# Performance work log

Measured on AMD Instinct MI355X. Metric: run time of the kernel, lower is better.

## Reference

```python
import jax, jax.numpy as jnp
import numpy as np

V, E, H, C, L, S, NL = 50257, 512, 1024, 1024, 1024, 2048, 2


def setup_inputs() -> dict:
    key = jax.random.key(0)
    ks = jax.random.split(key, 28)
    w = 0.02  # weight init scale
    def n(k, shape, s=1.0):
        return jax.random.normal(k, shape, dtype=jnp.float32) * s
    return {
        'input_ids': jax.random.randint(ks[0], (1,), 0, V, dtype=jnp.int32),
        'h0': n(ks[1], (NL, 1, H)),
        'c0': n(ks[2], (NL, 1, H)),
        'left_context': n(ks[3], (S, C)),
        'right_context': n(ks[4], (S, C)),
        'lemma_outputs': n(ks[5], (S, L)),
        # parameters
        'embedding': n(ks[6], (V, E), w),
        'W_ih0': n(ks[7], (4 * H, E), w), 'W_hh0': n(ks[8], (4 * H, H), w),
        'b_ih0': n(ks[9], (4 * H,), w), 'b_hh0': n(ks[10], (4 * H,), w),
        'W_ih1': n(ks[11], (4 * H, H), w), 'W_hh1': n(ks[12], (4 * H, H), w),
        'b_ih1': n(ks[13], (4 * H,), w), 'b_hh1': n(ks[14], (4 * H,), w),
        'W_left': n(ks[15], (H, C), w), 'b_left': n(ks[16], (H,), w),
        'W_right': n(ks[17], (H, C), w), 'b_right': n(ks[18], (H,), w),
        'W_lemma': n(ks[19], (H, L), w), 'b_lemma': n(ks[20], (H,), w),
        'W_concat': n(ks[21], (H, H + 2 * C + L), w), 'b_concat': n(ks[22], (H,), w),
        'W_out': n(ks[23], (V, H), w), 'b_out': n(ks[24], (V,), w),
    }


def _lstm_step(x, h, c, W_ih, W_hh, b_ih, b_hh):
    # torch LSTM gate order: i, f, g, o
    g = x @ W_ih.T + b_ih + h @ W_hh.T + b_hh  # [1, 4H]
    i, f, gg, o = jnp.split(g, 4, axis=-1)
    i = jax.nn.sigmoid(i); f = jax.nn.sigmoid(f)
    gg = jnp.tanh(gg); o = jax.nn.sigmoid(o)
    c_new = f * c + i * gg
    h_new = o * jnp.tanh(c_new)
    return h_new, c_new


def _attend(ctx, W, b, q):
    # ctx: [S, C], q: [1, H] -> Luong-style attention
    e = (ctx @ W.T + b) @ q.T          # [S, 1]
    a = jax.nn.softmax(e[:, 0])        # [S]
    return (a @ ctx)[None, :]          # [1, C]


def reference(input_ids, h0, c0, left_context, right_context, lemma_outputs,
              embedding, W_ih0, W_hh0, b_ih0, b_hh0, W_ih1, W_hh1, b_ih1, b_hh1,
              W_left, b_left, W_right, b_right, W_lemma, b_lemma,
              W_concat, b_concat, W_out, b_out):
    x = embedding[input_ids]  # [1, E]  (dropout p=0 -> identity)
    h_0, c_0 = _lstm_step(x, h0[0], c0[0], W_ih0, W_hh0, b_ih0, b_hh0)
    h_1, c_1 = _lstm_step(h_0, h0[1], c0[1], W_ih1, W_hh1, b_ih1, b_hh1)
    rnn_output = h_1  # [1, H]
    lcontext = _attend(left_context, W_left, b_left, rnn_output)
    rcontext = _attend(right_context, W_right, b_right, rnn_output)
    lemma_ctx = _attend(lemma_outputs, W_lemma, b_lemma, rnn_output)
    concat_in = jnp.concatenate([rnn_output, lcontext, rcontext, lemma_ctx], axis=-1)
    concat_out = jnp.tanh(concat_in @ W_concat.T + b_concat)  # [1, H]
    output = concat_out @ W_out.T + b_out                      # [1, V]
    h_new = jnp.stack([h_0, h_1], axis=0)  # [NL, 1, H]
    c_new = jnp.stack([c_0, c_1], axis=0)
    return output, h_new, c_new
```

## Files before the change

### kernel.cpp

```cpp
#include <hip/hip_runtime.h>
#include <hip/hip_bf16.h>
#include <math.h>


#define WS_H0        0
#define WS_CONCAT_IN 1024
#define WS_CTXOUT    2048
#define WS_V         5120
#define WS_E         8192
#define WS_COUT      20480
#define OUT_V        50257

__device__ __forceinline__ float wave_sum(float v) {
#pragma unroll
    for (int o = 32; o > 0; o >>= 1) v += __shfl_down(v, o, 64);
    return v;
}

__device__ __forceinline__ float dot4(float4 a, float4 b) {
    return a.x * b.x + a.y * b.y + a.z * b.z + a.w * b.w;
}

__device__ __forceinline__ float sigmoidf_(float x) {
    return 1.0f / (1.0f + expf(-x));
}

__global__ __launch_bounds__(256) void lstm_kernel(
    const float* __restrict__ x_base, const int* __restrict__ ids, int E_in,
    const float* __restrict__ W_ih, const float* __restrict__ W_hh,
    const float* __restrict__ b_ih, const float* __restrict__ b_hh,
    const float* __restrict__ hprev, const float* __restrict__ cprev,
    float* __restrict__ h_ws, float* __restrict__ h_out, float* __restrict__ c_out,
    float* __restrict__ zero_base, int zero_count)
{
    if (zero_base != nullptr) {
        int idx = blockIdx.x * 256 + threadIdx.x;
        if (idx < zero_count) zero_base[idx] = 0.0f;
    }

    const float* x = (ids != nullptr) ? (x_base + (size_t)512 * (size_t)ids[0]) : x_base;

    const int k = blockIdx.x;
    const int w = threadIdx.x >> 6;
    const int lane = threadIdx.x & 63;
    const int row = w * 1024 + k;

    float acc = 0.0f;
    {
        const float4* r4 = (const float4*)(W_ih + (size_t)row * E_in);
        const float4* x4 = (const float4*)x;
        const int n4 = E_in >> 2;
        for (int i = lane; i < n4; i += 64) acc += dot4(r4[i], x4[i]);
    }
    {
        const float4* r4 = (const float4*)(W_hh + (size_t)row * 1024);
        const float4* h4 = (const float4*)hprev;
        for (int i = lane; i < 256; i += 64) acc += dot4(r4[i], h4[i]);
    }
    acc = wave_sum(acc);

    __shared__ float g[4];
    if (lane == 0) g[w] = acc + b_ih[row] + b_hh[row];
    __syncthreads();
    if (threadIdx.x == 0) {
        float i_ = sigmoidf_(g[0]);
        float f_ = sigmoidf_(g[1]);
        float g_ = tanhf(g[2]);
        float o_ = sigmoidf_(g[3]);
        float c_new = f_ * cprev[k] + i_ * g_;
        float h_new = o_ * tanhf(c_new);
        h_ws[k] = h_new;
        h_out[k] = h_new;
        c_out[k] = c_new;
    }
}

__global__ __launch_bounds__(256) void attn_v_kernel(
    const float* __restrict__ W0, const float* __restrict__ W1,
    const float* __restrict__ W2, const float* __restrict__ q,
    float* __restrict__ v)
{
    const int a = blockIdx.x >> 6;
    const int chunk = blockIdx.x & 63;
    const float* W = (a == 0) ? W0 : (a == 1) ? W1 : W2;
    const int c = threadIdx.x * 4;
    float4 acc = make_float4(0.f, 0.f, 0.f, 0.f);
    const int h0 = chunk * 16;
#pragma unroll 4
    for (int h = h0; h < h0 + 16; ++h) {
        float qh = q[h];
        float4 wv = *(const float4*)(W + (size_t)h * 1024 + c);
        acc.x += wv.x * qh; acc.y += wv.y * qh;
        acc.z += wv.z * qh; acc.w += wv.w * qh;
    }
    float* vd = v + a * 1024 + c;
    atomicAdd(vd + 0, acc.x); atomicAdd(vd + 1, acc.y);
    atomicAdd(vd + 2, acc.z); atomicAdd(vd + 3, acc.w);
}

__global__ __launch_bounds__(256) void attn_e_kernel(
    const float* __restrict__ C0, const float* __restrict__ C1,
    const float* __restrict__ C2, const float* __restrict__ v,
    float* __restrict__ e)
{
    const int wid = (blockIdx.x * 256 + threadIdx.x) >> 6;
    const int lane = threadIdx.x & 63;
    if (wid >= 3 * 2048) return;
    const int a = wid >> 11;
    const int s = wid & 2047;
    const float* ctx = (a == 0) ? C0 : (a == 1) ? C1 : C2;
    const float4* r4 = (const float4*)(ctx + (size_t)s * 1024);
    const float4* v4 = (const float4*)(v + a * 1024);
    float acc = 0.0f;
    for (int i = lane; i < 256; i += 64) acc += dot4(r4[i], v4[i]);
    acc = wave_sum(acc);
    if (lane == 0) e[a * 2048 + s] = acc;
}

__global__ __launch_bounds__(256) void attn_ctx_kernel(
    const float* __restrict__ C0, const float* __restrict__ C1,
    const float* __restrict__ C2, const float* __restrict__ e,
    float* __restrict__ ctx_out)
{
    const int a = blockIdx.x >> 6;
    const int chunk = blockIdx.x & 63;
    const float* ctx = (a == 0) ? C0 : (a == 1) ? C1 : C2;
    const float* ea = e + a * 2048;

    __shared__ float red[256];
    const int t = threadIdx.x;
    float m = -1e30f;
    for (int i = t; i < 2048; i += 256) m = fmaxf(m, ea[i]);
    red[t] = m; __syncthreads();
    for (int o = 128; o > 0; o >>= 1) {
        if (t < o) red[t] = fmaxf(red[t], red[t + o]);
        __syncthreads();
    }
    m = red[0]; __syncthreads();

    float ssum = 0.0f;
    for (int i = t; i < 2048; i += 256) ssum += expf(ea[i] - m);
    red[t] = ssum; __syncthreads();
    for (int o = 128; o > 0; o >>= 1) {
        if (t < o) red[t] += red[t + o];
        __syncthreads();
    }
    const float inv = 1.0f / red[0];

    const int c = t * 4;
    float4 acc = make_float4(0.f, 0.f, 0.f, 0.f);
    const int s0 = chunk * 32;
    for (int s = s0; s < s0 + 32; ++s) {
        float wgt = expf(ea[s] - m) * inv;
        float4 cv = *(const float4*)(ctx + (size_t)s * 1024 + c);
        acc.x += wgt * cv.x; acc.y += wgt * cv.y;
        acc.z += wgt * cv.z; acc.w += wgt * cv.w;
    }
    float* od = ctx_out + a * 1024 + c;
    atomicAdd(od + 0, acc.x); atomicAdd(od + 1, acc.y);
    atomicAdd(od + 2, acc.z); atomicAdd(od + 3, acc.w);
}

__global__ __launch_bounds__(256) void concat_kernel(
    const float* __restrict__ W, const float* __restrict__ b,
    const float* __restrict__ cin, float* __restrict__ cout)
{
    const int w = threadIdx.x >> 6;
    const int lane = threadIdx.x & 63;
    const int j = blockIdx.x * 4 + w;
    const float4* r4 = (const float4*)(W + (size_t)j * 4096);
    const float4* x4 = (const float4*)cin;
    float acc = 0.0f;
    for (int i = lane; i < 1024; i += 64) acc += dot4(r4[i], x4[i]);
    acc = wave_sum(acc);
    if (lane == 0) cout[j] = tanhf(acc + b[j]);
}

__global__ __launch_bounds__(256) void out_kernel(
    const float* __restrict__ W, const float* __restrict__ b,
    const float* __restrict__ x, float* __restrict__ out)
{
    const int wid = (blockIdx.x * 256 + threadIdx.x) >> 6;
    const int lane = threadIdx.x & 63;
    const int nwaves = gridDim.x * 4;
    const float4* x4 = (const float4*)x;
    for (int vrow = wid; vrow < OUT_V; vrow += nwaves) {
        const float4* r4 = (const float4*)(W + (size_t)vrow * 1024);
        float acc = 0.0f;
        for (int i = lane; i < 256; i += 64) acc += dot4(r4[i], x4[i]);
        acc = wave_sum(acc);
        if (lane == 0) out[vrow] = acc + b[vrow];
    }
}

extern "C" void kernel_launch(void* const* d_in, const int* in_sizes, int n_in,
                              void* d_out, int out_size, void* d_ws, size_t ws_size,
                              hipStream_t stream) {
    const int*   input_ids = (const int*)  d_in[0];
    const float* h0        = (const float*)d_in[1];
    const float* c0        = (const float*)d_in[2];
    const float* lctx      = (const float*)d_in[3];
    const float* rctx      = (const float*)d_in[4];
    const float* lemma     = (const float*)d_in[5];
    const float* emb       = (const float*)d_in[6];
    const float* W_ih0     = (const float*)d_in[7];
    const float* W_hh0     = (const float*)d_in[8];
    const float* b_ih0     = (const float*)d_in[9];
    const float* b_hh0     = (const float*)d_in[10];
    const float* W_ih1     = (const float*)d_in[11];
    const float* W_hh1     = (const float*)d_in[12];
    const float* b_ih1     = (const float*)d_in[13];
    const float* b_hh1     = (const float*)d_in[14];
    const float* W_left    = (const float*)d_in[15];
    const float* b_left    = (const float*)d_in[16];
    const float* W_right   = (const float*)d_in[17];
    const float* W_lemma   = (const float*)d_in[19];
    const float* W_concat  = (const float*)d_in[21];
    const float* b_concat  = (const float*)d_in[22];
    const float* W_out     = (const float*)d_in[23];
    const float* b_out     = (const float*)d_in[24];
    (void)b_left; (void)in_sizes; (void)n_in; (void)out_size; (void)ws_size;

    float* out = (float*)d_out;
    float* ws  = (float*)d_ws;

    float* h0_out = out + OUT_V;
    float* h1_out = out + OUT_V + 1024;
    float* c0_out = out + OUT_V + 2048;
    float* c1_out = out + OUT_V + 3072;

    lstm_kernel<<<1024, 256, 0, stream>>>(
        emb, input_ids, 512, W_ih0, W_hh0, b_ih0, b_hh0,
        h0, c0, ws + WS_H0, h0_out, c0_out,
        ws + WS_CTXOUT, 6144 );

    lstm_kernel<<<1024, 256, 0, stream>>>(
        ws + WS_H0, nullptr, 1024, W_ih1, W_hh1, b_ih1, b_hh1,
        h0 + 1024, c0 + 1024, ws + WS_CONCAT_IN, h1_out, c1_out,
        nullptr, 0);

    attn_v_kernel<<<192, 256, 0, stream>>>(
        W_left, W_right, W_lemma, ws + WS_CONCAT_IN, ws + WS_V);

    attn_e_kernel<<<1536, 256, 0, stream>>>(
        lctx, rctx, lemma, ws + WS_V, ws + WS_E);

    attn_ctx_kernel<<<192, 256, 0, stream>>>(
        lctx, rctx, lemma, ws + WS_E, ws + WS_CTXOUT);

    concat_kernel<<<256, 256, 0, stream>>>(
        W_concat, b_concat, ws + WS_CONCAT_IN, ws + WS_COUT);

    out_kernel<<<2048, 256, 0, stream>>>(
        W_out, b_out, ws + WS_COUT, out);
}
```

Measured before the change: 466.0 us.

## Fuse all decoder stages into one cooperative persistent kernel with grid syncs

```diff
diff --git a/kernel.cpp b/kernel.cpp
--- a/kernel.cpp
+++ b/kernel.cpp
@@ -1,15 +1,23 @@
 #include <hip/hip_runtime.h>
 #include <hip/hip_bf16.h>
+#include <hip/hip_cooperative_groups.h>
 #include <math.h>
 
-
-#define WS_H0        0
-#define WS_CONCAT_IN 1024
-#define WS_CTXOUT    2048
-#define WS_V         5120
-#define WS_E         8192
-#define WS_COUT      20480
-#define OUT_V        50257
+namespace cg = cooperative_groups;
+
+
+#define NV 50257
+#define GRID 512
+
+struct Params {
+    const int* ids;
+    const float *h0, *c0, *lctx, *rctx, *lemma, *emb;
+    const float *W_ih0, *W_hh0, *b_ih0, *b_hh0;
+    const float *W_ih1, *W_hh1, *b_ih1, *b_hh1;
+    const float *W_left, *W_right, *W_lemma;
+    const float *W_concat, *b_concat, *W_out, *b_out;
+    float *out, *ws;
+};
 
 __device__ __forceinline__ float wave_sum(float v) {
 #pragma unroll
@@ -25,232 +33,244 @@
     return 1.0f / (1.0f + expf(-x));
 }
 
-__global__ __launch_bounds__(256) void lstm_kernel(
-    const float* __restrict__ x_base, const int* __restrict__ ids, int E_in,
-    const float* __restrict__ W_ih, const float* __restrict__ W_hh,
-    const float* __restrict__ b_ih, const float* __restrict__ b_hh,
-    const float* __restrict__ hprev, const float* __restrict__ cprev,
-    float* __restrict__ h_ws, float* __restrict__ h_out, float* __restrict__ c_out,
-    float* __restrict__ zero_base, int zero_count)
-{
-    if (zero_base != nullptr) {
-        int idx = blockIdx.x * 256 + threadIdx.x;
-        if (idx < zero_count) zero_base[idx] = 0.0f;
-    }
-
-    const float* x = (ids != nullptr) ? (x_base + (size_t)512 * (size_t)ids[0]) : x_base;
-
-    const int k = blockIdx.x;
-    const int w = threadIdx.x >> 6;
-    const int lane = threadIdx.x & 63;
-    const int row = w * 1024 + k;
-
-    float acc = 0.0f;
-    {
-        const float4* r4 = (const float4*)(W_ih + (size_t)row * E_in);
-        const float4* x4 = (const float4*)x;
-        const int n4 = E_in >> 2;
-        for (int i = lane; i < n4; i += 64) acc += dot4(r4[i], x4[i]);
-    }
-    {
-        const float4* r4 = (const float4*)(W_hh + (size_t)row * 1024);
-        const float4* h4 = (const float4*)hprev;
-        for (int i = lane; i < 256; i += 64) acc += dot4(r4[i], h4[i]);
-    }
-    acc = wave_sum(acc);
+__global__ __launch_bounds__(256, 2) void fused_decoder(Params p) {
+    cg::grid_group grid = cg::this_grid();
+    const int bid  = blockIdx.x;
+    const int tid  = threadIdx.x;
+    const int w    = tid >> 6;
+    const int lane = tid & 63;
+
+    float* h0_ws = p.ws;
+    float* cin   = p.ws + 1024;
+    float* vbuf  = p.ws + 5120;
+    float* ebuf  = p.ws + 8192;
+    float* cout  = p.ws + 14336;
+    float* h_out = p.out + NV;
+    float* c_out = p.out + NV + 2048;
 
     __shared__ float g[4];
-    if (lane == 0) g[w] = acc + b_ih[row] + b_hh[row];
-    __syncthreads();
-    if (threadIdx.x == 0) {
-        float i_ = sigmoidf_(g[0]);
-        float f_ = sigmoidf_(g[1]);
-        float g_ = tanhf(g[2]);
-        float o_ = sigmoidf_(g[3]);
-        float c_new = f_ * cprev[k] + i_ * g_;
-        float h_new = o_ * tanhf(c_new);
-        h_ws[k] = h_new;
-        h_out[k] = h_new;
-        c_out[k] = c_new;
-    }
-}
-
-__global__ __launch_bounds__(256) void attn_v_kernel(
-    const float* __restrict__ W0, const float* __restrict__ W1,
-    const float* __restrict__ W2, const float* __restrict__ q,
-    float* __restrict__ v)
-{
-    const int a = blockIdx.x >> 6;
-    const int chunk = blockIdx.x & 63;
-    const float* W = (a == 0) ? W0 : (a == 1) ? W1 : W2;
-    const int c = threadIdx.x * 4;
-    float4 acc = make_float4(0.f, 0.f, 0.f, 0.f);
-    const int h0 = chunk * 16;
+    __shared__ float red[256];
+
+    if (bid < 24) {
+        p.ws[2048 + bid * 256 + tid] = 0.0f;
+    }
+    {
+        const float* x = p.emb + (size_t)512 * (size_t)p.ids[0];
+        for (int k = bid; k < 1024; k += GRID) {
+            const int row = w * 1024 + k;
+            float acc = 0.0f;
+            {
+                const float4* r4 = (const float4*)(p.W_ih0 + (size_t)row * 512);
+                const float4* x4 = (const float4*)x;
+#pragma unroll
+                for (int j = 0; j < 2; ++j) acc += dot4(r4[lane + 64 * j], x4[lane + 64 * j]);
+            }
+            {
+                const float4* r4 = (const float4*)(p.W_hh0 + (size_t)row * 1024);
+                const float4* h4 = (const float4*)p.h0;
+#pragma unroll
+                for (int j = 0; j < 4; ++j) acc += dot4(r4[lane + 64 * j], h4[lane + 64 * j]);
+            }
+            acc = wave_sum(acc);
+            if (lane == 0) g[w] = acc + p.b_ih0[row] + p.b_hh0[row];
+            __syncthreads();
+            if (tid == 0) {
+                float i_ = sigmoidf_(g[0]);
+                float f_ = sigmoidf_(g[1]);
+                float g_ = tanhf(g[2]);
+                float o_ = sigmoidf_(g[3]);
+                float c_new = f_ * p.c0[k] + i_ * g_;
+                float h_new = o_ * tanhf(c_new);
+                h0_ws[k]  = h_new;
+                h_out[k]  = h_new;
+                c_out[k]  = c_new;
+            }
+            __syncthreads();
+        }
+    }
+    grid.sync();
+
+    {
+        for (int k = bid; k < 1024; k += GRID) {
+            const int row = w * 1024 + k;
+            float acc = 0.0f;
+            {
+                const float4* r4 = (const float4*)(p.W_ih1 + (size_t)row * 1024);
+                const float4* x4 = (const float4*)h0_ws;
+#pragma unroll
+                for (int j = 0; j < 4; ++j) acc += dot4(r4[lane + 64 * j], x4[lane + 64 * j]);
+            }
+            {
+                const float4* r4 = (const float4*)(p.W_hh1 + (size_t)row * 1024);
+                const float4* h4 = (const float4*)(p.h0 + 1024);
+#pragma unroll
+                for (int j = 0; j < 4; ++j) acc += dot4(r4[lane + 64 * j], h4[lane + 64 * j]);
+            }
+            acc = wave_sum(acc);
+            if (lane == 0) g[w] = acc + p.b_ih1[row] + p.b_hh1[row];
+            __syncthreads();
+            if (tid == 0) {
+                float i_ = sigmoidf_(g[0]);
+                float f_ = sigmoidf_(g[1]);
+                float g_ = tanhf(g[2]);
+                float o_ = sigmoidf_(g[3]);
+                float c_new = f_ * p.c0[1024 + k] + i_ * g_;
+                float h_new = o_ * tanhf(c_new);
+                cin[k]          = h_new;
+                h_out[1024 + k] = h_new;
+                c_out[1024 + k] = c_new;
+            }
+            __syncthreads();
+        }
+    }
+    grid.sync();
+
+    if (bid < 192) {
+        const int a = bid >> 6;
+        const int chunk = bid & 63;
+        const float* W = (a == 0) ? p.W_left : (a == 1) ? p.W_right : p.W_lemma;
+        const int c = tid * 4;
+        float4 acc = make_float4(0.f, 0.f, 0.f, 0.f);
 #pragma unroll 4
-    for (int h = h0; h < h0 + 16; ++h) {
-        float qh = q[h];
-        float4 wv = *(const float4*)(W + (size_t)h * 1024 + c);
-        acc.x += wv.x * qh; acc.y += wv.y * qh;
-        acc.z += wv.z * qh; acc.w += wv.w * qh;
-    }
-    float* vd = v + a * 1024 + c;
-    atomicAdd(vd + 0, acc.x); atomicAdd(vd + 1, acc.y);
-    atomicAdd(vd + 2, acc.z); atomicAdd(vd + 3, acc.w);
-}
-
-__global__ __launch_bounds__(256) void attn_e_kernel(
-    const float* __restrict__ C0, const float* __restrict__ C1,
-    const float* __restrict__ C2, const float* __restrict__ v,
-    float* __restrict__ e)
-{
-    const int wid = (blockIdx.x * 256 + threadIdx.x) >> 6;
-    const int lane = threadIdx.x & 63;
-    if (wid >= 3 * 2048) return;
-    const int a = wid >> 11;
-    const int s = wid & 2047;
-    const float* ctx = (a == 0) ? C0 : (a == 1) ? C1 : C2;
-    const float4* r4 = (const float4*)(ctx + (size_t)s * 1024);
-    const float4* v4 = (const float4*)(v + a * 1024);
-    float acc = 0.0f;
-    for (int i = lane; i < 256; i += 64) acc += dot4(r4[i], v4[i]);
-    acc = wave_sum(acc);
-    if (lane == 0) e[a * 2048 + s] = acc;
-}
-
-__global__ __launch_bounds__(256) void attn_ctx_kernel(
-    const float* __restrict__ C0, const float* __restrict__ C1,
-    const float* __restrict__ C2, const float* __restrict__ e,
-    float* __restrict__ ctx_out)
-{
-    const int a = blockIdx.x >> 6;
-    const int chunk = blockIdx.x & 63;
-    const float* ctx = (a == 0) ? C0 : (a == 1) ? C1 : C2;
-    const float* ea = e + a * 2048;
-
-    __shared__ float red[256];
-    const int t = threadIdx.x;
-    float m = -1e30f;
-    for (int i = t; i < 2048; i += 256) m = fmaxf(m, ea[i]);
-    red[t] = m; __syncthreads();
-    for (int o = 128; o > 0; o >>= 1) {
-        if (t < o) red[t] = fmaxf(red[t], red[t + o]);
-        __syncthreads();
-    }
-    m = red[0]; __syncthreads();
-
-    float ssum = 0.0f;
-    for (int i = t; i < 2048; i += 256) ssum += expf(ea[i] - m);
-    red[t] = ssum; __syncthreads();
-    for (int o = 128; o > 0; o >>= 1) {
-        if (t < o) red[t] += red[t + o];
-        __syncthreads();
-    }
-    const float inv = 1.0f / red[0];
-
-    const int c = t * 4;
-    float4 acc = make_float4(0.f, 0.f, 0.f, 0.f);
-    const int s0 = chunk * 32;
-    for (int s = s0; s < s0 + 32; ++s) {
-        float wgt = expf(ea[s] - m) * inv;
-        float4 cv = *(const float4*)(ctx + (size_t)s * 1024 + c);
-        acc.x += wgt * cv.x; acc.y += wgt * cv.y;
-        acc.z += wgt * cv.z; acc.w += wgt * cv.w;
-    }
-    float* od = ctx_out + a * 1024 + c;
-    atomicAdd(od + 0, acc.x); atomicAdd(od + 1, acc.y);
-    atomicAdd(od + 2, acc.z); atomicAdd(od + 3, acc.w);
-}
-
-__global__ __launch_bounds__(256) void concat_kernel(
-    const float* __restrict__ W, const float* __restrict__ b,
-    const float* __restrict__ cin, float* __restrict__ cout)
-{
-    const int w = threadIdx.x >> 6;
-    const int lane = threadIdx.x & 63;
-    const int j = blockIdx.x * 4 + w;
-    const float4* r4 = (const float4*)(W + (size_t)j * 4096);
-    const float4* x4 = (const float4*)cin;
-    float acc = 0.0f;
-    for (int i = lane; i < 1024; i += 64) acc += dot4(r4[i], x4[i]);
-    acc = wave_sum(acc);
-    if (lane == 0) cout[j] = tanhf(acc + b[j]);
-}
-
-__global__ __launch_bounds__(256) void out_kernel(
-    const float* __restrict__ W, const float* __restrict__ b,
-    const float* __restrict__ x, float* __restrict__ out)
-{
-    const int wid = (blockIdx.x * 256 + threadIdx.x) >> 6;
-    const int lane = threadIdx.x & 63;
-    const int nwaves = gridDim.x * 4;
-    const float4* x4 = (const float4*)x;
-    for (int vrow = wid; vrow < OUT_V; vrow += nwaves) {
-        const float4* r4 = (const float4*)(W + (size_t)vrow * 1024);
+        for (int h = chunk * 16; h < chunk * 16 + 16; ++h) {
+            float qh = cin[h];
+            float4 wv = *(const float4*)(W + (size_t)h * 1024 + c);
+            acc.x += wv.x * qh; acc.y += wv.y * qh;
+            acc.z += wv.z * qh; acc.w += wv.w * qh;
+        }
+        float* vd = vbuf + a * 1024 + c;
+        atomicAdd(vd + 0, acc.x); atomicAdd(vd + 1, acc.y);
+        atomicAdd(vd + 2, acc.z); atomicAdd(vd + 3, acc.w);
+    }
+    grid.sync();
+
+    {
+        const int wid = bid * 4 + w;
+        for (int rr = wid; rr < 6144; rr += GRID * 4) {
+            const int a = rr >> 11;
+            const int s = rr & 2047;
+            const float* ctx = (a == 0) ? p.lctx : (a == 1) ? p.rctx : p.lemma;
+            const float4* r4 = (const float4*)(ctx + (size_t)s * 1024);
+            const float4* v4 = (const float4*)(vbuf + a * 1024);
+            float acc = 0.0f;
+#pragma unroll
+            for (int j = 0; j < 4; ++j) acc += dot4(r4[lane + 64 * j], v4[lane + 64 * j]);
+            acc = wave_sum(acc);
+            if (lane == 0) ebuf[rr] = acc;
+        }
+    }
+    grid.sync();
+
+    if (bid < 192) {
+        const int a = bid >> 6;
+        const int chunk = bid & 63;
+        const float* ctx = (a == 0) ? p.lctx : (a == 1) ? p.rctx : p.lemma;
+        const float* ea = ebuf + a * 2048;
+
+        float m = -1e30f;
+        for (int i = tid; i < 2048; i += 256) m = fmaxf(m, ea[i]);
+        red[tid] = m; __syncthreads();
+        for (int o = 128; o > 0; o >>= 1) {
+            if (tid < o) red[tid] = fmaxf(red[tid], red[tid + o]);
+            __syncthreads();
+        }
+        m = red[0]; __syncthreads();
+
+        float ssum = 0.0f;
+        for (int i = tid; i < 2048; i += 256) ssum += expf(ea[i] - m);
+        red[tid] = ssum; __syncthreads();
+        for (int o = 128; o > 0; o >>= 1) {
+            if (tid < o) red[tid] += red[tid + o];
+            __syncthreads();
+        }
+        const float inv = 1.0f / red[0];
+
+        const int c = tid * 4;
+        float4 acc = make_float4(0.f, 0.f, 0.f, 0.f);
+        for (int s = chunk * 32; s < chunk * 32 + 32; ++s) {
+            float wgt = expf(ea[s] - m) * inv;
+            float4 cv = *(const float4*)(ctx + (size_t)s * 1024 + c);
+            acc.x += wgt * cv.x; acc.y += wgt * cv.y;
+            acc.z += wgt * cv.z; acc.w += wgt * cv.w;
+        }
+        float* od = cin + 1024 + a * 1024 + c;
+        atomicAdd(od + 0, acc.x); atomicAdd(od + 1, acc.y);
+        atomicAdd(od + 2, acc.z); atomicAdd(od + 3, acc.w);
+    }
+    grid.sync();
+
+    if (bid < 256) {
+        const int j = bid * 4 + w;
+        const float4* r4 = (const float4*)(p.W_concat + (size_t)j * 4096);
+        const float4* x4 = (const float4*)cin;
         float acc = 0.0f;
-        for (int i = lane; i < 256; i += 64) acc += dot4(r4[i], x4[i]);
+#pragma unroll 4
+        for (int i = lane; i < 1024; i += 64) acc += dot4(r4[i], x4[i]);
         acc = wave_sum(acc);
-        if (lane == 0) out[vrow] = acc + b[vrow];
+        if (lane == 0) cout[j] = tanhf(acc + p.b_concat[j]);
+    }
+    grid.sync();
+
+    {
+        const int wid = bid * 4 + w;
+        const int stride = GRID * 4;
+        const float4* x4 = (const float4*)cout;
+        const float4 xr0 = x4[lane];
+        const float4 xr1 = x4[lane + 64];
+        const float4 xr2 = x4[lane + 128];
+        const float4 xr3 = x4[lane + 192];
+        for (int vr0 = wid; vr0 < NV; vr0 += 2 * stride) {
+            const int vr1 = vr0 + stride;
+            const float4* r0 = (const float4*)(p.W_out + (size_t)vr0 * 1024);
+            float acc0 = dot4(r0[lane], xr0) + dot4(r0[lane + 64], xr1)
+                       + dot4(r0[lane + 128], xr2) + dot4(r0[lane + 192], xr3);
+            float acc1 = 0.0f;
+            if (vr1 < NV) {
+                const float4* r1 = (const float4*)(p.W_out + (size_t)vr1 * 1024);
+                acc1 = dot4(r1[lane], xr0) + dot4(r1[lane + 64], xr1)
+                     + dot4(r1[lane + 128], xr2) + dot4(r1[lane + 192], xr3);
+            }
+            acc0 = wave_sum(acc0);
+            acc1 = wave_sum(acc1);
+            if (lane == 0) {
+                p.out[vr0] = acc0 + p.b_out[vr0];
+                if (vr1 < NV) p.out[vr1] = acc1 + p.b_out[vr1];
+            }
+        }
     }
 }
 
 extern "C" void kernel_launch(void* const* d_in, const int* in_sizes, int n_in,
                               void* d_out, int out_size, void* d_ws, size_t ws_size,
                               hipStream_t stream) {
-    const int*   input_ids = (const int*)  d_in[0];
-    const float* h0        = (const float*)d_in[1];
-    const float* c0        = (const float*)d_in[2];
-    const float* lctx      = (const float*)d_in[3];
-    const float* rctx      = (const float*)d_in[4];
-    const float* lemma     = (const float*)d_in[5];
-    const float* emb       = (const float*)d_in[6];
-    const float* W_ih0     = (const float*)d_in[7];
-    const float* W_hh0     = (const float*)d_in[8];
-    const float* b_ih0     = (const float*)d_in[9];
-    const float* b_hh0     = (const float*)d_in[10];
-    const float* W_ih1     = (const float*)d_in[11];
-    const float* W_hh1     = (const float*)d_in[12];
-    const float* b_ih1     = (const float*)d_in[13];
-    const float* b_hh1     = (const float*)d_in[14];
-    const float* W_left    = (const float*)d_in[15];
-    const float* b_left    = (const float*)d_in[16];
-    const float* W_right   = (const float*)d_in[17];
-    const float* W_lemma   = (const float*)d_in[19];
-    const float* W_concat  = (const float*)d_in[21];
-    const float* b_concat  = (const float*)d_in[22];
-    const float* W_out     = (const float*)d_in[23];
-    const float* b_out     = (const float*)d_in[24];
-    (void)b_left; (void)in_sizes; (void)n_in; (void)out_size; (void)ws_size;
-
-    float* out = (float*)d_out;
-    float* ws  = (float*)d_ws;
-
-    float* h0_out = out + OUT_V;
-    float* h1_out = out + OUT_V + 1024;
-    float* c0_out = out + OUT_V + 2048;
-    float* c1_out = out + OUT_V + 3072;
-
-    lstm_kernel<<<1024, 256, 0, stream>>>(
-        emb, input_ids, 512, W_ih0, W_hh0, b_ih0, b_hh0,
-        h0, c0, ws + WS_H0, h0_out, c0_out,
-        ws + WS_CTXOUT, 6144 );
-
-    lstm_kernel<<<1024, 256, 0, stream>>>(
-        ws + WS_H0, nullptr, 1024, W_ih1, W_hh1, b_ih1, b_hh1,
-        h0 + 1024, c0 + 1024, ws + WS_CONCAT_IN, h1_out, c1_out,
-        nullptr, 0);
-
-    attn_v_kernel<<<192, 256, 0, stream>>>(
-        W_left, W_right, W_lemma, ws + WS_CONCAT_IN, ws + WS_V);
-
-    attn_e_kernel<<<1536, 256, 0, stream>>>(
-        lctx, rctx, lemma, ws + WS_V, ws + WS_E);
-
-    attn_ctx_kernel<<<192, 256, 0, stream>>>(
-        lctx, rctx, lemma, ws + WS_E, ws + WS_CTXOUT);
-
-    concat_kernel<<<256, 256, 0, stream>>>(
-        W_concat, b_concat, ws + WS_CONCAT_IN, ws + WS_COUT);
-
-    out_kernel<<<2048, 256, 0, stream>>>(
-        W_out, b_out, ws + WS_COUT, out);
-}
+    Params p;
+    p.ids      = (const int*)  d_in[0];
+    p.h0       = (const float*)d_in[1];
+    p.c0       = (const float*)d_in[2];
+    p.lctx     = (const float*)d_in[3];
+    p.rctx     = (const float*)d_in[4];
+    p.lemma    = (const float*)d_in[5];
+    p.emb      = (const float*)d_in[6];
+    p.W_ih0    = (const float*)d_in[7];
+    p.W_hh0    = (const float*)d_in[8];
+    p.b_ih0    = (const float*)d_in[9];
+    p.b_hh0    = (const float*)d_in[10];
+    p.W_ih1    = (const float*)d_in[11];
+    p.W_hh1    = (const float*)d_in[12];
+    p.b_ih1    = (const float*)d_in[13];
+    p.b_hh1    = (const float*)d_in[14];
+    p.W_left   = (const float*)d_in[15];
+    p.W_right  = (const float*)d_in[17];
+    p.W_lemma  = (const float*)d_in[19];
+    p.W_concat = (const float*)d_in[21];
+    p.b_concat = (const float*)d_in[22];
+    p.W_out    = (const float*)d_in[23];
+    p.b_out    = (const float*)d_in[24];
+    p.out      = (float*)d_out;
+    p.ws       = (float*)d_ws;
+    (void)in_sizes; (void)n_in; (void)out_size; (void)ws_size;
+
+    void* args[] = { &p };
+    hipLaunchCooperativeKernel((void*)fused_decoder, dim3(GRID), dim3(256),
+                               args, 0, stream);
+}
```

Result: slower. 819.9 us (+75.9%).
